# Performance work log

Hardware: AMD Instinct MI355X
Metric: run time of the kernel (lower is better)

Reference implementation:

```python
import jax, jax.numpy as jnp
import numpy as np

K = 3  # kernel size
PAD = 1
C_IN = 32
C_OUT = 32
CKK = C_IN * K * K  # 288
HID = C_OUT  # hidden width of kernel-generator MLP


def _unfold(x):
    """torch F.unfold equivalent, (C, kh, kw)-major. x: [B,C,H,W] -> [B, C*K*K, H*W]."""
    B, C, H, W = x.shape
    xp = jnp.pad(x, ((0, 0), (0, 0), (PAD, PAD), (PAD, PAD)))
    # stack K*K shifted views -> [B, C, K*K, H, W]
    patches = jnp.stack(
        [xp[:, :, i:i + H, j:j + W] for i in range(K) for j in range(K)], axis=2
    )
    return patches.reshape(B, C * K * K, H * W)


def setup_inputs() -> dict:
    key = jax.random.key(0)
    ks = jax.random.split(key, 6)
    B, H, W = 2, 64, 64
    x = jax.random.normal(ks[0], (B, C_IN, H, W), dtype=jnp.float32)
    # kernel_generator: Linear(CKK -> HID), Tanh, Linear(HID -> C_OUT*CKK)
    s1 = 1.0 / np.sqrt(CKK)
    s2 = 1.0 / np.sqrt(HID)
    W1 = jax.random.uniform(ks[1], (HID, CKK), jnp.float32, -s1, s1)
    b1 = jax.random.uniform(ks[2], (HID,), jnp.float32, -s1, s1)
    W2 = jax.random.uniform(ks[3], (C_OUT * CKK, HID), jnp.float32, -s2, s2)
    b2 = jax.random.uniform(ks[4], (C_OUT * CKK,), jnp.float32, -s2, s2)
    bias = jax.random.uniform(ks[5], (C_OUT,), jnp.float32, -s1, s1)
    return {"x": x, "W1": W1, "b1": b1, "W2": W2, "b2": b2, "bias": bias}


def reference(x, W1, b1, W2, b2, bias):
    B, C, H, W = x.shape
    L = H * W
    u = _unfold(x)                       # [B, CKK, L]
    ut = u.transpose(0, 2, 1)            # [B, L, CKK]
    h = jnp.tanh(jnp.einsum('blj,hj->blh', ut, W1) + b1)          # [B, L, HID]
    kern = jnp.einsum('blh,oh->blo', h, W2) + b2                  # [B, L, C_OUT*CKK]
    kern = kern.reshape(B, L, C_OUT, CKK)                         # per-pixel kernels
    out = jnp.einsum('bloj,blj->bol', kern, ut)                   # [B, C_OUT, L]
    out = out.reshape(B, C_OUT, H, W) + bias[None, :, None, None]
    return out
```

## Files before the change

### kernel.cpp

```cpp
#include <hip/hip_runtime.h>
#include <hip/hip_bf16.h>


#define CKK 288
#define SJ  296

typedef __attribute__((ext_vector_type(8))) short short8;
typedef __attribute__((ext_vector_type(4))) float f32x4;

#define W2B_OFF 0
#define W1B_OFF 294912
#define B2B_OFF (294912 + 9216)
#define WS_ELEMS (294912 + 9216 + 9216)

__global__ __launch_bounds__(256) void prep_kernel(
    const float* __restrict__ W1, const float* __restrict__ W2,
    const float* __restrict__ b2, __hip_bfloat16* __restrict__ ws)
{
    int idx = blockIdx.x * 256 + threadIdx.x;
    if (idx < 294912) {
        int n = idx / CKK, j = idx - n * CKK;
        int o = n >> 5, h = n & 31;
        ws[W2B_OFF + idx] = __float2bfloat16(W2[(o * CKK + j) * 32 + h]);
    } else if (idx < 294912 + 9216) {
        int k = idx - 294912;
        ws[W1B_OFF + k] = __float2bfloat16(W1[k]);
    } else if (idx < WS_ELEMS) {
        int k = idx - (294912 + 9216);
        ws[B2B_OFF + k] = __float2bfloat16(b2[k]);
    }
}

__global__ __launch_bounds__(512) void dynaconv_main(
    const float* __restrict__ x,
    const float* __restrict__ b1,
    const float* __restrict__ bias,
    const __hip_bfloat16* __restrict__ ws,
    float* __restrict__ out)
{
    __shared__ __hip_bfloat16 u_lds[32 * SJ];
    __shared__ float hh_lds[32 * 33];
    __shared__ float o_lds[32 * 33];

    const int t  = threadIdx.x;
    const int w  = t >> 6;
    const int l  = t & 63;
    const int lg = l >> 4;
    const int lr = l & 15;

    const int g0  = blockIdx.x * 32;
    const int b   = g0 >> 12;
    const int l0  = g0 & 4095;
    const int y   = l0 >> 6;
    const int wx0 = l0 & 63;

    #pragma unroll
    for (int k = 0; k < 18; ++k) {
        int idx = k * 512 + t;
        int j = idx >> 5, p = idx & 31;
        int c = j / 9, r = j - c * 9;
        int ki = r / 3, kj = r - ki * 3;
        int y2 = y + ki - 1;
        int x2 = wx0 + p + kj - 1;
        float v = 0.f;
        if ((unsigned)y2 < 64u && (unsigned)x2 < 64u)
            v = x[((b * 32 + c) * 64 + y2) * 64 + x2];
        u_lds[p * SJ + j] = __float2bfloat16(v);
    }
    __syncthreads();

    if (w < 4) {
        const __hip_bfloat16* Bmat = ws + ((w < 2) ? B2B_OFF : W1B_OFF);
        const int col = ((w & 1) * 16) + lr;
        f32x4 acc0 = {0.f, 0.f, 0.f, 0.f}, acc1 = {0.f, 0.f, 0.f, 0.f};
        #pragma unroll
        for (int kb = 0; kb < 9; ++kb) {
            short8 bf = *(const short8*)(Bmat + col * CKK + kb * 32 + lg * 8);
            short8 a0 = *(const short8*)(u_lds + lr * SJ + kb * 32 + lg * 8);
            short8 a1 = *(const short8*)(u_lds + (16 + lr) * SJ + kb * 32 + lg * 8);
            acc0 = __builtin_amdgcn_mfma_f32_16x16x32_bf16(a0, bf, acc0, 0, 0, 0);
            acc1 = __builtin_amdgcn_mfma_f32_16x16x32_bf16(a1, bf, acc1, 0, 0, 0);
        }
        if (w < 2) {
            float bv = bias[col];
            #pragma unroll
            for (int r = 0; r < 4; ++r) {
                o_lds[(lg * 4 + r) * 33 + col]        = acc0[r] + bv;
                o_lds[(16 + lg * 4 + r) * 33 + col]   = acc1[r] + bv;
            }
        } else {
            float b1v = b1[col];
            #pragma unroll
            for (int r = 0; r < 4; ++r) {
                hh_lds[(lg * 4 + r) * 33 + col]       = tanhf(acc0[r] + b1v);
                hh_lds[(16 + lg * 4 + r) * 33 + col]  = tanhf(acc1[r] + b1v);
            }
        }
    }
    __syncthreads();

    f32x4 acc[2][8];
    #pragma unroll
    for (int m = 0; m < 2; ++m)
        #pragma unroll
        for (int nf = 0; nf < 8; ++nf)
            acc[m][nf] = f32x4{0.f, 0.f, 0.f, 0.f};

    {
        const __hip_bfloat16* W2b = ws + W2B_OFF;
        const int nbase = w * 128;
        short8 bcur[8];
        #pragma unroll
        for (int nf = 0; nf < 8; ++nf)
            bcur[nf] = *(const short8*)(W2b + (size_t)(nbase + nf * 16 + lr) * CKK + lg * 8);

        #pragma unroll
        for (int kb = 0; kb < 9; ++kb) {
            short8 a0 = *(const short8*)(u_lds + lr * SJ + kb * 32 + lg * 8);
            short8 a1 = *(const short8*)(u_lds + (16 + lr) * SJ + kb * 32 + lg * 8);
            short8 bnext[8];
            if (kb < 8) {
                #pragma unroll
                for (int nf = 0; nf < 8; ++nf)
                    bnext[nf] = *(const short8*)(W2b + (size_t)(nbase + nf * 16 + lr) * CKK
                                                 + (kb + 1) * 32 + lg * 8);
            }
            #pragma unroll
            for (int nf = 0; nf < 8; ++nf) {
                acc[0][nf] = __builtin_amdgcn_mfma_f32_16x16x32_bf16(a0, bcur[nf], acc[0][nf], 0, 0, 0);
                acc[1][nf] = __builtin_amdgcn_mfma_f32_16x16x32_bf16(a1, bcur[nf], acc[1][nf], 0, 0, 0);
            }
            if (kb < 8) {
                #pragma unroll
                for (int nf = 0; nf < 8; ++nf)
                    bcur[nf] = bnext[nf];
            }
        }
    }

    #pragma unroll
    for (int ol = 0; ol < 4; ++ol) {
        const int o = w * 4 + ol;
        #pragma unroll
        for (int m = 0; m < 2; ++m) {
            #pragma unroll
            for (int r = 0; r < 4; ++r) {
                const int p = m * 16 + lg * 4 + r;
                float v = hh_lds[p * 33 + lr]      * acc[m][ol * 2][r]
                        + hh_lds[p * 33 + 16 + lr] * acc[m][ol * 2 + 1][r];
                v += __shfl_xor(v, 1);
                v += __shfl_xor(v, 2);
                v += __shfl_xor(v, 4);
                v += __shfl_xor(v, 8);
                if (lr == 0) o_lds[p * 33 + o] += v;
            }
        }
    }
    __syncthreads();

    #pragma unroll
    for (int k = 0; k < 2; ++k) {
        int idx = k * 512 + t;
        int o = idx >> 5, p = idx & 31;
        out[((size_t)(b * 32 + o)) * 4096 + l0 + p] = o_lds[p * 33 + o];
    }
}

extern "C" void kernel_launch(void* const* d_in, const int* in_sizes, int n_in,
                              void* d_out, int out_size, void* d_ws, size_t ws_size,
                              hipStream_t stream) {
    const float* x    = (const float*)d_in[0];
    const float* W1   = (const float*)d_in[1];
    const float* b1   = (const float*)d_in[2];
    const float* W2   = (const float*)d_in[3];
    const float* b2   = (const float*)d_in[4];
    const float* bias = (const float*)d_in[5];
    float* out = (float*)d_out;
    __hip_bfloat16* ws = (__hip_bfloat16*)d_ws;

    prep_kernel<<<(WS_ELEMS + 255) / 256, 256, 0, stream>>>(W1, W2, b2, ws);
    dynaconv_main<<<256, 512, 0, stream>>>(x, b1, bias, ws, out);
}
```

Measured before the change: 32.51 us.

## Split into unfold/MLP kernel and output-channel-tiled GEMM kernel with LDS-staged patches

Restructures the pipeline into two kernels. The first does the bf16 W2 conversion, W1/b2 staging into LDS, patch unfold, the hidden layer and the b2 term, and writes swizzled patches, tanh activations and partial outputs to workspace. The second tiles work as 256 pixels by 4 output channels, keeps the W2 slice in registers, and double-buffers patch tiles into LDS with global_load_lds. The aim is to stop every block from streaming all of W2, at the cost of extra workspace round-trips and a reduced-intensity second GEMM.

```diff
diff --git a/kernel.cpp b/kernel.cpp
--- a/kernel.cpp
+++ b/kernel.cpp
@@ -9,50 +9,50 @@
 typedef __attribute__((ext_vector_type(4))) float f32x4;
 
 #define W2B_OFF 0
-#define W1B_OFF 294912
-#define B2B_OFF (294912 + 9216)
-#define WS_ELEMS (294912 + 9216 + 9216)
-
-__global__ __launch_bounds__(256) void prep_kernel(
-    const float* __restrict__ W1, const float* __restrict__ W2,
-    const float* __restrict__ b2, __hip_bfloat16* __restrict__ ws)
+#define U_OFF   294912
+#define U_ELEMS (9 * 8192 * 32)
+#define HH_BYTE ((U_OFF + U_ELEMS) * 2)
+#define T_BYTE  (HH_BYTE + 8192 * 32 * 4)
+
+__global__ __launch_bounds__(512) void dynaconv_up(
+    const float* __restrict__ x, const float* __restrict__ W1,
+    const float* __restrict__ b1, const float* __restrict__ W2,
+    const float* __restrict__ b2, const float* __restrict__ bias,
+    char* __restrict__ wsraw)
 {
-    int idx = blockIdx.x * 256 + threadIdx.x;
-    if (idx < 294912) {
-        int n = idx / CKK, j = idx - n * CKK;
-        int o = n >> 5, h = n & 31;
-        ws[W2B_OFF + idx] = __float2bfloat16(W2[(o * CKK + j) * 32 + h]);
-    } else if (idx < 294912 + 9216) {
-        int k = idx - 294912;
-        ws[W1B_OFF + k] = __float2bfloat16(W1[k]);
-    } else if (idx < WS_ELEMS) {
-        int k = idx - (294912 + 9216);
-        ws[B2B_OFF + k] = __float2bfloat16(b2[k]);
-    }
-}
-
-__global__ __launch_bounds__(512) void dynaconv_main(
-    const float* __restrict__ x,
-    const float* __restrict__ b1,
-    const float* __restrict__ bias,
-    const __hip_bfloat16* __restrict__ ws,
-    float* __restrict__ out)
-{
-    __shared__ __hip_bfloat16 u_lds[32 * SJ];
-    __shared__ float hh_lds[32 * 33];
-    __shared__ float o_lds[32 * 33];
+    __hip_bfloat16* wsb = (__hip_bfloat16*)wsraw;
+    float* hh_ws = (float*)(wsraw + HH_BYTE);
+    float* t_ws  = (float*)(wsraw + T_BYTE);
+
+    __shared__ __align__(16) __hip_bfloat16 u_lds[32 * SJ];
+    __shared__ __align__(16) __hip_bfloat16 w1_lds[32 * SJ];
+    __shared__ __align__(16) __hip_bfloat16 b2_lds[32 * SJ];
 
     const int t  = threadIdx.x;
-    const int w  = t >> 6;
-    const int l  = t & 63;
-    const int lg = l >> 4;
-    const int lr = l & 15;
-
-    const int g0  = blockIdx.x * 32;
-    const int b   = g0 >> 12;
-    const int l0  = g0 & 4095;
-    const int y   = l0 >> 6;
-    const int wx0 = l0 & 63;
+    const int w  = t >> 6, l = t & 63, lg = l >> 4, lr = l & 15;
+    const int g0 = blockIdx.x * 32;
+    const int b  = g0 >> 12, l0 = g0 & 4095, y = l0 >> 6, wx0 = l0 & 63;
+
+    {
+        int gid = blockIdx.x * 512 + t;
+        #pragma unroll
+        for (int k = 0; k < 3; ++k) {
+            int idx = k * 131072 + gid;
+            if (idx < 294912) {
+                int n = idx / CKK, j = idx - n * CKK;
+                int o = n >> 5, h = n & 31;
+                wsb[W2B_OFF + idx] = __float2bfloat16(W2[(o * CKK + j) * 32 + h]);
+            }
+        }
+    }
+
+    #pragma unroll
+    for (int k = 0; k < 18; ++k) {
+        int idx = k * 512 + t;
+        int row = idx / CKK, jj = idx - row * CKK;
+        w1_lds[row * SJ + jj] = __float2bfloat16(W1[idx]);
+        b2_lds[row * SJ + jj] = __float2bfloat16(b2[idx]);
+    }
 
     #pragma unroll
     for (int k = 0; k < 18; ++k) {
@@ -60,8 +60,7 @@
         int j = idx >> 5, p = idx & 31;
         int c = j / 9, r = j - c * 9;
         int ki = r / 3, kj = r - ki * 3;
-        int y2 = y + ki - 1;
-        int x2 = wx0 + p + kj - 1;
+        int y2 = y + ki - 1, x2 = wx0 + p + kj - 1;
         float v = 0.f;
         if ((unsigned)y2 < 64u && (unsigned)x2 < 64u)
             v = x[((b * 32 + c) * 64 + y2) * 64 + x2];
@@ -69,13 +68,31 @@
     }
     __syncthreads();
 
+    {
+        const int mt  = blockIdx.x >> 3;
+        const int rf0 = (blockIdx.x * 2) & 15;
+        #pragma unroll
+        for (int k = 0; k < 3; ++k) {
+            int idx = k * 512 + t;
+            if (idx < 1152) {
+                int kb = idx >> 7, rem = idx & 127;
+                int rfl = rem >> 6, ll = rem & 63;
+                int p = rfl * 16 + (ll & 15);
+                int j = kb * 32 + ((ll >> 4) << 3);
+                short8 v = *(const short8*)(u_lds + p * SJ + j);
+                int dst16 = ((kb * 32 + mt) * 16 + rf0 + rfl) * 64 + ll;
+                *(short8*)(wsb + U_OFF + dst16 * 8) = v;
+            }
+        }
+    }
+
     if (w < 4) {
-        const __hip_bfloat16* Bmat = ws + ((w < 2) ? B2B_OFF : W1B_OFF);
-        const int col = ((w & 1) * 16) + lr;
-        f32x4 acc0 = {0.f, 0.f, 0.f, 0.f}, acc1 = {0.f, 0.f, 0.f, 0.f};
+        const __hip_bfloat16* Bl = (w < 2) ? b2_lds : w1_lds;
+        const int col = (w & 1) * 16 + lr;
+        f32x4 acc0 = {0.f,0.f,0.f,0.f}, acc1 = {0.f,0.f,0.f,0.f};
         #pragma unroll
         for (int kb = 0; kb < 9; ++kb) {
-            short8 bf = *(const short8*)(Bmat + col * CKK + kb * 32 + lg * 8);
+            short8 bf = *(const short8*)(Bl + col * SJ + kb * 32 + lg * 8);
             short8 a0 = *(const short8*)(u_lds + lr * SJ + kb * 32 + lg * 8);
             short8 a1 = *(const short8*)(u_lds + (16 + lr) * SJ + kb * 32 + lg * 8);
             acc0 = __builtin_amdgcn_mfma_f32_16x16x32_bf16(a0, bf, acc0, 0, 0, 0);
@@ -85,75 +102,111 @@
             float bv = bias[col];
             #pragma unroll
             for (int r = 0; r < 4; ++r) {
-                o_lds[(lg * 4 + r) * 33 + col]        = acc0[r] + bv;
-                o_lds[(16 + lg * 4 + r) * 33 + col]   = acc1[r] + bv;
+                t_ws[col * 8192 + g0 + lg * 4 + r]      = acc0[r] + bv;
+                t_ws[col * 8192 + g0 + 16 + lg * 4 + r] = acc1[r] + bv;
             }
         } else {
             float b1v = b1[col];
             #pragma unroll
             for (int r = 0; r < 4; ++r) {
-                hh_lds[(lg * 4 + r) * 33 + col]       = tanhf(acc0[r] + b1v);
-                hh_lds[(16 + lg * 4 + r) * 33 + col]  = tanhf(acc1[r] + b1v);
-            }
-        }
-    }
+                hh_ws[(g0 + lg * 4 + r) * 32 + col]      = tanhf(acc0[r] + b1v);
+                hh_ws[(g0 + 16 + lg * 4 + r) * 32 + col] = tanhf(acc1[r] + b1v);
+            }
+        }
+    }
+}
+
+__device__ __forceinline__ void stage_a(const __hip_bfloat16* __restrict__ src,
+                                        __hip_bfloat16* dst, int w, int l)
+{
+    #pragma unroll
+    for (int c = 0; c < 2; ++c) {
+        const __hip_bfloat16* g = src + (w * 128 + c * 64 + l) * 8;
+        __hip_bfloat16* s = dst + (w * 128 + c * 64) * 8;
+        __builtin_amdgcn_global_load_lds(
+            (const __attribute__((address_space(1))) void*)g,
+            (__attribute__((address_space(3))) void*)s, 16, 0, 0);
+    }
+}
+
+__global__ __launch_bounds__(512) void dynaconv_g(
+    const char* __restrict__ wsraw, float* __restrict__ out)
+{
+    const __hip_bfloat16* W2b  = (const __hip_bfloat16*)wsraw;
+    const __hip_bfloat16* u_ws = (const __hip_bfloat16*)wsraw + U_OFF;
+    const float* hh_ws = (const float*)(wsraw + HH_BYTE);
+    const float* t_ws  = (const float*)(wsraw + T_BYTE);
+
+    __shared__ __align__(16) __hip_bfloat16 abuf[2][8192];
+    __shared__ float hh_lds[256 * 34];
+    __shared__ float o_lds[256 * 5];
+
+    const int t = threadIdx.x;
+    const int w = t >> 6, l = t & 63, lg = l >> 4, lr = l & 15;
+    const int mw = w >> 2, nw = w & 3;
+    const int mtile = blockIdx.x >> 3, ntile = blockIdx.x & 7;
+    const int m0 = mtile * 256, o0 = ntile * 4;
+    const int o = o0 + nw;
+
+    short8 breg[9][2];
+    #pragma unroll
+    for (int kb = 0; kb < 9; ++kb)
+        #pragma unroll
+        for (int nf = 0; nf < 2; ++nf) {
+            int n = o * 32 + nf * 16 + lr;
+            breg[kb][nf] = *(const short8*)(W2b + n * CKK + kb * 32 + lg * 8);
+        }
+
+    #pragma unroll
+    for (int k = 0; k < 4; ++k) {
+        int idx = k * 512 + t;
+        int p = idx >> 3, h4 = (idx & 7) * 4;
+        f32x4 v = *(const f32x4*)(hh_ws + (m0 + p) * 32 + h4);
+        hh_lds[p * 34 + h4 + 0] = v[0];
+        hh_lds[p * 34 + h4 + 1] = v[1];
+        hh_lds[p * 34 + h4 + 2] = v[2];
+        hh_lds[p * 34 + h4 + 3] = v[3];
+    }
+
+    stage_a(u_ws + (0 * 32 + mtile) * 8192, &abuf[0][0], w, l);
     __syncthreads();
 
-    f32x4 acc[2][8];
-    #pragma unroll
-    for (int m = 0; m < 2; ++m)
-        #pragma unroll
-        for (int nf = 0; nf < 8; ++nf)
-            acc[m][nf] = f32x4{0.f, 0.f, 0.f, 0.f};
-
-    {
-        const __hip_bfloat16* W2b = ws + W2B_OFF;
-        const int nbase = w * 128;
-        short8 bcur[8];
-        #pragma unroll
-        for (int nf = 0; nf < 8; ++nf)
-            bcur[nf] = *(const short8*)(W2b + (size_t)(nbase + nf * 16 + lr) * CKK + lg * 8);
-
-        #pragma unroll
-        for (int kb = 0; kb < 9; ++kb) {
-            short8 a0 = *(const short8*)(u_lds + lr * SJ + kb * 32 + lg * 8);
-            short8 a1 = *(const short8*)(u_lds + (16 + lr) * SJ + kb * 32 + lg * 8);
-            short8 bnext[8];
-            if (kb < 8) {
-                #pragma unroll
-                for (int nf = 0; nf < 8; ++nf)
-                    bnext[nf] = *(const short8*)(W2b + (size_t)(nbase + nf * 16 + lr) * CKK
-                                                 + (kb + 1) * 32 + lg * 8);
-            }
-            #pragma unroll
-            for (int nf = 0; nf < 8; ++nf) {
-                acc[0][nf] = __builtin_amdgcn_mfma_f32_16x16x32_bf16(a0, bcur[nf], acc[0][nf], 0, 0, 0);
-                acc[1][nf] = __builtin_amdgcn_mfma_f32_16x16x32_bf16(a1, bcur[nf], acc[1][nf], 0, 0, 0);
-            }
-            if (kb < 8) {
-                #pragma unroll
-                for (int nf = 0; nf < 8; ++nf)
-                    bcur[nf] = bnext[nf];
-            }
-        }
-    }
-
-    #pragma unroll
-    for (int ol = 0; ol < 4; ++ol) {
-        const int o = w * 4 + ol;
-        #pragma unroll
-        for (int m = 0; m < 2; ++m) {
-            #pragma unroll
-            for (int r = 0; r < 4; ++r) {
-                const int p = m * 16 + lg * 4 + r;
-                float v = hh_lds[p * 33 + lr]      * acc[m][ol * 2][r]
-                        + hh_lds[p * 33 + 16 + lr] * acc[m][ol * 2 + 1][r];
-                v += __shfl_xor(v, 1);
-                v += __shfl_xor(v, 2);
-                v += __shfl_xor(v, 4);
-                v += __shfl_xor(v, 8);
-                if (lr == 0) o_lds[p * 33 + o] += v;
-            }
+    f32x4 acc[8][2];
+    #pragma unroll
+    for (int mf = 0; mf < 8; ++mf) {
+        acc[mf][0] = f32x4{0.f,0.f,0.f,0.f};
+        acc[mf][1] = f32x4{0.f,0.f,0.f,0.f};
+    }
+
+    #pragma unroll
+    for (int kb = 0; kb < 9; ++kb) {
+        const int cur = kb & 1;
+        if (kb < 8)
+            stage_a(u_ws + ((kb + 1) * 32 + mtile) * 8192, &abuf[cur ^ 1][0], w, l);
+        short8 a[8];
+        #pragma unroll
+        for (int mf = 0; mf < 8; ++mf)
+            a[mf] = *(const short8*)(&abuf[cur][((mw * 8 + mf) * 64 + l) * 8]);
+        #pragma unroll
+        for (int mf = 0; mf < 8; ++mf) {
+            acc[mf][0] = __builtin_amdgcn_mfma_f32_16x16x32_bf16(a[mf], breg[kb][0], acc[mf][0], 0, 0, 0);
+            acc[mf][1] = __builtin_amdgcn_mfma_f32_16x16x32_bf16(a[mf], breg[kb][1], acc[mf][1], 0, 0, 0);
+        }
+        __syncthreads();
+    }
+
+    #pragma unroll
+    for (int mf = 0; mf < 8; ++mf) {
+        #pragma unroll
+        for (int r = 0; r < 4; ++r) {
+            int p = mw * 128 + mf * 16 + lg * 4 + r;
+            float v = hh_lds[p * 34 + lr]      * acc[mf][0][r]
+                    + hh_lds[p * 34 + 16 + lr] * acc[mf][1][r];
+            v += __shfl_xor(v, 1);
+            v += __shfl_xor(v, 2);
+            v += __shfl_xor(v, 4);
+            v += __shfl_xor(v, 8);
+            if (lr == 0) o_lds[p * 5 + nw] = v;
         }
     }
     __syncthreads();
@@ -161,8 +214,11 @@
     #pragma unroll
     for (int k = 0; k < 2; ++k) {
         int idx = k * 512 + t;
-        int o = idx >> 5, p = idx & 31;
-        out[((size_t)(b * 32 + o)) * 4096 + l0 + p] = o_lds[p * 33 + o];
+        int oj = idx >> 8, p = idx & 255;
+        int gp = m0 + p;
+        float val = o_lds[p * 5 + oj] + t_ws[(o0 + oj) * 8192 + gp];
+        int bb = gp >> 12;
+        out[((size_t)(bb * 32 + o0 + oj)) * 4096 + (gp & 4095)] = val;
     }
 }
 
@@ -176,8 +232,8 @@
     const float* b2   = (const float*)d_in[4];
     const float* bias = (const float*)d_in[5];
     float* out = (float*)d_out;
-    __hip_bfloat16* ws = (__hip_bfloat16*)d_ws;
-
-    prep_kernel<<<(WS_ELEMS + 255) / 256, 256, 0, stream>>>(W1, W2, b2, ws);
-    dynaconv_main<<<256, 512, 0, stream>>>(x, b1, bias, ws, out);
-}
+    char* ws = (char*)d_ws;
+
+    dynaconv_up<<<256, 512, 0, stream>>>(x, W1, b1, W2, b2, bias, ws);
+    dynaconv_g<<<256, 512, 0, stream>>>(ws, out);
+}
```

Result: slower. 37.78 us (+16.2%).

## Fuse weight prep into single kernel with register-resident W2 slices per output tile

Applied to the files above, without the earlier changes.

Removes the separate bf16 weight-conversion kernel and launches one fused kernel. Each block owns four output channels, keeps its W2 slice (converted on the fly from strided fp32 loads) in registers, and loops over two image rows that are staged in LDS before the unfold. The aim is to cut the extra launch and the repeated W2 streaming from global memory. In exchange every block re-reads and converts W2 with uncoalesced strided loads, and the kernel now needs many more registers.

```diff
diff --git a/kernel.cpp b/kernel.cpp
--- a/kernel.cpp
+++ b/kernel.cpp
@@ -6,163 +6,179 @@
 #define SJ  296
 
 typedef __attribute__((ext_vector_type(8))) short short8;
+typedef __attribute__((ext_vector_type(4))) short short4v;
 typedef __attribute__((ext_vector_type(4))) float f32x4;
 
-#define W2B_OFF 0
-#define W1B_OFF 294912
-#define B2B_OFF (294912 + 9216)
-#define WS_ELEMS (294912 + 9216 + 9216)
-
-__global__ __launch_bounds__(256) void prep_kernel(
-    const float* __restrict__ W1, const float* __restrict__ W2,
-    const float* __restrict__ b2, __hip_bfloat16* __restrict__ ws)
-{
-    int idx = blockIdx.x * 256 + threadIdx.x;
-    if (idx < 294912) {
-        int n = idx / CKK, j = idx - n * CKK;
-        int o = n >> 5, h = n & 31;
-        ws[W2B_OFF + idx] = __float2bfloat16(W2[(o * CKK + j) * 32 + h]);
-    } else if (idx < 294912 + 9216) {
-        int k = idx - 294912;
-        ws[W1B_OFF + k] = __float2bfloat16(W1[k]);
-    } else if (idx < WS_ELEMS) {
-        int k = idx - (294912 + 9216);
-        ws[B2B_OFF + k] = __float2bfloat16(b2[k]);
-    }
+__device__ __forceinline__ short f2bf(float f) {
+    __hip_bfloat16 h = __float2bfloat16(f);
+    return __builtin_bit_cast(short, h);
 }
 
-__global__ __launch_bounds__(512) void dynaconv_main(
+__global__ __launch_bounds__(256, 2) void dynaconv_one(
     const float* __restrict__ x,
+    const float* __restrict__ W1,
     const float* __restrict__ b1,
+    const float* __restrict__ W2,
+    const float* __restrict__ b2,
     const float* __restrict__ bias,
-    const __hip_bfloat16* __restrict__ ws,
     float* __restrict__ out)
 {
-    __shared__ __hip_bfloat16 u_lds[32 * SJ];
-    __shared__ float hh_lds[32 * 33];
-    __shared__ float o_lds[32 * 33];
+    __shared__ __align__(16) float x_lds[3][32][66];
+    __shared__ __align__(16) __hip_bfloat16 u_lds[64 * SJ];
+    __shared__ float hh_lds[64 * 33];
+    __shared__ float t_lds[64 * 4];
+    __shared__ float o_stage[4][64];
 
     const int t  = threadIdx.x;
-    const int w  = t >> 6;
-    const int l  = t & 63;
-    const int lg = l >> 4;
-    const int lr = l & 15;
+    const int w  = t >> 6, l = t & 63, lg = l >> 4, lr = l & 15;
+    const int nt = blockIdx.x & 7, mt = blockIdx.x >> 3;
+    const int o_w = nt * 4 + w;
 
-    const int g0  = blockIdx.x * 32;
-    const int b   = g0 >> 12;
-    const int l0  = g0 & 4095;
-    const int y   = l0 >> 6;
-    const int wx0 = l0 & 63;
-
+    short8 breg[9][2];
     #pragma unroll
-    for (int k = 0; k < 18; ++k) {
-        int idx = k * 512 + t;
-        int j = idx >> 5, p = idx & 31;
-        int c = j / 9, r = j - c * 9;
-        int ki = r / 3, kj = r - ki * 3;
-        int y2 = y + ki - 1;
-        int x2 = wx0 + p + kj - 1;
-        float v = 0.f;
-        if ((unsigned)y2 < 64u && (unsigned)x2 < 64u)
-            v = x[((b * 32 + c) * 64 + y2) * 64 + x2];
-        u_lds[p * SJ + j] = __float2bfloat16(v);
-    }
-    __syncthreads();
-
-    if (w < 4) {
-        const __hip_bfloat16* Bmat = ws + ((w < 2) ? B2B_OFF : W1B_OFF);
-        const int col = ((w & 1) * 16) + lr;
-        f32x4 acc0 = {0.f, 0.f, 0.f, 0.f}, acc1 = {0.f, 0.f, 0.f, 0.f};
+    for (int nf = 0; nf < 2; ++nf) {
+        const int h = nf * 16 + lr;
+        const size_t base = (size_t)o_w * CKK * 32 + h;
         #pragma unroll
         for (int kb = 0; kb < 9; ++kb) {
-            short8 bf = *(const short8*)(Bmat + col * CKK + kb * 32 + lg * 8);
-            short8 a0 = *(const short8*)(u_lds + lr * SJ + kb * 32 + lg * 8);
-            short8 a1 = *(const short8*)(u_lds + (16 + lr) * SJ + kb * 32 + lg * 8);
-            acc0 = __builtin_amdgcn_mfma_f32_16x16x32_bf16(a0, bf, acc0, 0, 0, 0);
-            acc1 = __builtin_amdgcn_mfma_f32_16x16x32_bf16(a1, bf, acc1, 0, 0, 0);
+            short8 v;
+            #pragma unroll
+            for (int i = 0; i < 8; ++i) {
+                int j = kb * 32 + lg * 8 + i;
+                v[i] = f2bf(W2[base + (size_t)j * 32]);
+            }
+            breg[kb][nf] = v;
         }
+    }
+    short8 ereg[9];
+    if (w < 2) {
+        const int h = w * 16 + lr;
+        #pragma unroll
+        for (int kb = 0; kb < 9; ++kb) {
+            short8 v;
+            #pragma unroll
+            for (int i = 0; i < 8; ++i)
+                v[i] = f2bf(W1[h * CKK + kb * 32 + lg * 8 + i]);
+            ereg[kb] = v;
+        }
+    } else if (w == 2) {
+        #pragma unroll
+        for (int kb = 0; kb < 9; ++kb) {
+            short8 v;
+            #pragma unroll
+            for (int i = 0; i < 8; ++i) {
+                float f = (lr < 4) ? b2[(nt * 4 + lr) * CKK + kb * 32 + lg * 8 + i] : 0.f;
+                v[i] = f2bf(f);
+            }
+            ereg[kb] = v;
+        }
+    } else {
+        #pragma unroll
+        for (int kb = 0; kb < 9; ++kb) ereg[kb] = short8{0,0,0,0,0,0,0,0};
+    }
+
+    for (int sub = 0; sub < 2; ++sub) {
+        const int row = mt * 2 + sub;
+        const int b   = row >> 6;
+        const int y   = row & 63;
+
+        __syncthreads();
+        #pragma unroll
+        for (int k = 0; k < 24; ++k) {
+            int idx = k * 256 + t;
+            int ky  = idx >> 11;
+            int rem = idx & 2047;
+            int c   = rem >> 6;
+            int wx  = rem & 63;
+            int yy  = y + ky - 1;
+            float v = 0.f;
+            if ((unsigned)yy < 64u)
+                v = x[((b * 32 + c) * 64 + yy) * 64 + wx];
+            x_lds[ky][c][wx + 1] = v;
+        }
+        if (t < 96) {
+            int ky = t / 32, c = t & 31;
+            x_lds[ky][c][0]  = 0.f;
+            x_lds[ky][c][65] = 0.f;
+        }
+        __syncthreads();
+
+        {
+            const int p = t & 63, jq = t >> 6;
+            #pragma unroll
+            for (int j4 = 0; j4 < 18; ++j4) {
+                short4v sv;
+                #pragma unroll
+                for (int e = 0; e < 4; ++e) {
+                    int j  = jq * 72 + j4 * 4 + e;
+                    int c  = j / 9, r = j - c * 9;
+                    int ki = r / 3, kj = r - ki * 3;
+                    sv[e] = f2bf(x_lds[ki][c][p + kj]);
+                }
+                *(short4v*)(u_lds + p * SJ + jq * 72 + j4 * 4) = sv;
+            }
+        }
+        __syncthreads();
+
+        f32x4 acc[4][2], acce[4];
+        #pragma unroll
+        for (int mf = 0; mf < 4; ++mf) {
+            acc[mf][0] = f32x4{0.f,0.f,0.f,0.f};
+            acc[mf][1] = f32x4{0.f,0.f,0.f,0.f};
+            acce[mf]   = f32x4{0.f,0.f,0.f,0.f};
+        }
+        #pragma unroll
+        for (int kb = 0; kb < 9; ++kb) {
+            short8 a[4];
+            #pragma unroll
+            for (int mf = 0; mf < 4; ++mf)
+                a[mf] = *(const short8*)(u_lds + (mf * 16 + lr) * SJ + kb * 32 + lg * 8);
+            #pragma unroll
+            for (int mf = 0; mf < 4; ++mf) {
+                acc[mf][0] = __builtin_amdgcn_mfma_f32_16x16x32_bf16(a[mf], breg[kb][0], acc[mf][0], 0, 0, 0);
+                acc[mf][1] = __builtin_amdgcn_mfma_f32_16x16x32_bf16(a[mf], breg[kb][1], acc[mf][1], 0, 0, 0);
+            }
+            if (w < 3) {
+                #pragma unroll
+                for (int mf = 0; mf < 4; ++mf)
+                    acce[mf] = __builtin_amdgcn_mfma_f32_16x16x32_bf16(a[mf], ereg[kb], acce[mf], 0, 0, 0);
+            }
+        }
+
         if (w < 2) {
-            float bv = bias[col];
+            const int h = w * 16 + lr;
+            const float b1v = b1[h];
+            #pragma unroll
+            for (int mf = 0; mf < 4; ++mf)
+                #pragma unroll
+                for (int r = 0; r < 4; ++r)
+                    hh_lds[(mf * 16 + lg * 4 + r) * 33 + h] = tanhf(acce[mf][r] + b1v);
+        } else if (w == 2 && lr < 4) {
+            const float bv = bias[nt * 4 + lr];
+            #pragma unroll
+            for (int mf = 0; mf < 4; ++mf)
+                #pragma unroll
+                for (int r = 0; r < 4; ++r)
+                    t_lds[(mf * 16 + lg * 4 + r) * 4 + lr] = acce[mf][r] + bv;
+        }
+        __syncthreads();
+
+        #pragma unroll
+        for (int mf = 0; mf < 4; ++mf) {
             #pragma unroll
             for (int r = 0; r < 4; ++r) {
-                o_lds[(lg * 4 + r) * 33 + col]        = acc0[r] + bv;
-                o_lds[(16 + lg * 4 + r) * 33 + col]   = acc1[r] + bv;
-            }
-        } else {
-            float b1v = b1[col];
-            #pragma unroll
-            for (int r = 0; r < 4; ++r) {
-                hh_lds[(lg * 4 + r) * 33 + col]       = tanhf(acc0[r] + b1v);
-                hh_lds[(16 + lg * 4 + r) * 33 + col]  = tanhf(acc1[r] + b1v);
-            }
-        }
-    }
-    __syncthreads();
-
-    f32x4 acc[2][8];
-    #pragma unroll
-    for (int m = 0; m < 2; ++m)
-        #pragma unroll
-        for (int nf = 0; nf < 8; ++nf)
-            acc[m][nf] = f32x4{0.f, 0.f, 0.f, 0.f};
-
-    {
-        const __hip_bfloat16* W2b = ws + W2B_OFF;
-        const int nbase = w * 128;
-        short8 bcur[8];
-        #pragma unroll
-        for (int nf = 0; nf < 8; ++nf)
-            bcur[nf] = *(const short8*)(W2b + (size_t)(nbase + nf * 16 + lr) * CKK + lg * 8);
-
-        #pragma unroll
-        for (int kb = 0; kb < 9; ++kb) {
-            short8 a0 = *(const short8*)(u_lds + lr * SJ + kb * 32 + lg * 8);
-            short8 a1 = *(const short8*)(u_lds + (16 + lr) * SJ + kb * 32 + lg * 8);
-            short8 bnext[8];
-            if (kb < 8) {
-                #pragma unroll
-                for (int nf = 0; nf < 8; ++nf)
-                    bnext[nf] = *(const short8*)(W2b + (size_t)(nbase + nf * 16 + lr) * CKK
-                                                 + (kb + 1) * 32 + lg * 8);
-            }
-            #pragma unroll
-            for (int nf = 0; nf < 8; ++nf) {
-                acc[0][nf] = __builtin_amdgcn_mfma_f32_16x16x32_bf16(a0, bcur[nf], acc[0][nf], 0, 0, 0);
-                acc[1][nf] = __builtin_amdgcn_mfma_f32_16x16x32_bf16(a1, bcur[nf], acc[1][nf], 0, 0, 0);
-            }
-            if (kb < 8) {
-                #pragma unroll
-                for (int nf = 0; nf < 8; ++nf)
-                    bcur[nf] = bnext[nf];
-            }
-        }
-    }
-
-    #pragma unroll
-    for (int ol = 0; ol < 4; ++ol) {
-        const int o = w * 4 + ol;
-        #pragma unroll
-        for (int m = 0; m < 2; ++m) {
-            #pragma unroll
-            for (int r = 0; r < 4; ++r) {
-                const int p = m * 16 + lg * 4 + r;
-                float v = hh_lds[p * 33 + lr]      * acc[m][ol * 2][r]
-                        + hh_lds[p * 33 + 16 + lr] * acc[m][ol * 2 + 1][r];
+                const int p = mf * 16 + lg * 4 + r;
+                float v = hh_lds[p * 33 + lr]      * acc[mf][0][r]
+                        + hh_lds[p * 33 + 16 + lr] * acc[mf][1][r];
                 v += __shfl_xor(v, 1);
                 v += __shfl_xor(v, 2);
                 v += __shfl_xor(v, 4);
                 v += __shfl_xor(v, 8);
-                if (lr == 0) o_lds[p * 33 + o] += v;
+                if (lr == 0) o_stage[w][p] = v;
             }
         }
-    }
-    __syncthreads();
-
-    #pragma unroll
-    for (int k = 0; k < 2; ++k) {
-        int idx = k * 512 + t;
-        int o = idx >> 5, p = idx & 31;
-        out[((size_t)(b * 32 + o)) * 4096 + l0 + p] = o_lds[p * 33 + o];
+        float res = o_stage[w][l] + t_lds[l * 4 + w];
+        out[((size_t)(b * 32 + o_w)) * 4096 + y * 64 + l] = res;
     }
 }
 
@@ -176,8 +192,6 @@
     const float* b2   = (const float*)d_in[4];
     const float* bias = (const float*)d_in[5];
     float* out = (float*)d_out;
-    __hip_bfloat16* ws = (__hip_bfloat16*)d_ws;
 
-    prep_kernel<<<(WS_ELEMS + 255) / 256, 256, 0, stream>>>(W1, W2, b2, ws);
-    dynaconv_main<<<256, 512, 0, stream>>>(x, b1, bias, ws, out);
+    dynaconv_one<<<512, 256, 0, stream>>>(x, W1, b1, W2, b2, bias, out);
 }
```

New measurement: 60.33 us. 85.6% more time.
